# Performance work log

Hardware: AMD Instinct MI355X
Metric: run time of the kernel (lower is better)

The kernel has to match this reference:

```python
import jax, jax.numpy as jnp
import numpy as np

B, L, D, H, UNITS = 64, 4096, 512, 512, 256

def setup_inputs() -> dict:
    key = jax.random.key(0)
    ks = jax.random.split(key, 8)
    s = lambda fan_in: 1.0 / np.sqrt(fan_in)
    return {
        "features": jax.random.normal(ks[0], (B, L, D), dtype=jnp.float32),
        "hidden": jax.random.normal(ks[1], (B, H), dtype=jnp.float32),
        "W1_k": jax.random.uniform(ks[2], (D, UNITS), jnp.float32, -s(D), s(D)),
        "W1_b": jnp.zeros((UNITS,), jnp.float32),
        "W2_k": jax.random.uniform(ks[3], (H, UNITS), jnp.float32, -s(H), s(H)),
        "W2_b": jnp.zeros((UNITS,), jnp.float32),
        "V_k": jax.random.uniform(ks[4], (UNITS, 1), jnp.float32, -s(UNITS), s(UNITS)),
        "V_b": jnp.zeros((1,), jnp.float32),
    }

def reference(features, hidden, W1_k, W1_b, W2_k, W2_b, V_k, V_b):
    # features: [B, L, D], hidden: [B, H]
    f_proj = jnp.einsum('bld,du->blu', features, W1_k) + W1_b          # [B, L, U]
    h_proj = (hidden @ W2_k + W2_b)[:, None, :]                        # [B, 1, U]
    score = jnp.einsum('blu,uo->blo', jnp.tanh(f_proj + h_proj), V_k) + V_b  # [B, L, 1]
    attention_weights = jax.nn.softmax(score, axis=1)                  # [B, L, 1]
    context_vector = jnp.sum(attention_weights * features, axis=1)     # [B, D]
    return (context_vector, attention_weights)
```

## Files before the change

### kernel.cpp

```cpp
#include <hip/hip_runtime.h>

#define Bsz 64
#define Lsz 4096
#define Dsz 512
#define Hsz 512
#define Usz 256
#define LT  64
#define NLB (Lsz / LT)
#define AW  520

typedef __attribute__((ext_vector_type(8))) short s8v;
typedef __attribute__((ext_vector_type(4))) float f4v;
typedef __attribute__((ext_vector_type(8))) unsigned short u16x8;

__device__ __forceinline__ unsigned short f2bf(float f) {
    unsigned int u = __float_as_uint(f);
    u += 0x7FFFu + ((u >> 16) & 1u);
    return (unsigned short)(u >> 16);
}
__device__ __forceinline__ float bf2f(unsigned int lo16) {
    return __uint_as_float(lo16 << 16);
}


__global__ __launch_bounds__(256) void k_prep(const float* __restrict__ W1,
                                              const float* __restrict__ hidden,
                                              const float* __restrict__ W2,
                                              unsigned short* __restrict__ W1T,
                                              float* __restrict__ hp_part,
                                              float* __restrict__ den,
                                              float* __restrict__ ctx_acc) {
    int blk = blockIdx.x, tid = threadIdx.x;
    if (blk < 32) {
        __shared__ unsigned short Lt[64][72];
        int kb = blk >> 2, ub = blk & 3;
        {
            int rr = tid >> 2, c16 = (tid & 3) * 16;
            const float* src = W1 + (size_t)(kb * 64 + rr) * Usz + ub * 64 + c16;
            f4v v0 = *reinterpret_cast<const f4v*>(src);
            f4v v1 = *reinterpret_cast<const f4v*>(src + 4);
            f4v v2 = *reinterpret_cast<const f4v*>(src + 8);
            f4v v3 = *reinterpret_cast<const f4v*>(src + 12);
            u16x8 o0 = { f2bf(v0.x), f2bf(v0.y), f2bf(v0.z), f2bf(v0.w),
                         f2bf(v1.x), f2bf(v1.y), f2bf(v1.z), f2bf(v1.w) };
            u16x8 o1 = { f2bf(v2.x), f2bf(v2.y), f2bf(v2.z), f2bf(v2.w),
                         f2bf(v3.x), f2bf(v3.y), f2bf(v3.z), f2bf(v3.w) };
            *reinterpret_cast<u16x8*>(&Lt[rr][c16])     = o0;
            *reinterpret_cast<u16x8*>(&Lt[rr][c16 + 8]) = o1;
        }
        __syncthreads();
        {
            int ur = tid >> 2, k16 = (tid & 3) * 16;
            u16x8 o0, o1;
#pragma unroll
            for (int i = 0; i < 8; ++i) o0[i] = Lt[k16 + i][ur];
#pragma unroll
            for (int i = 0; i < 8; ++i) o1[i] = Lt[k16 + 8 + i][ur];
            unsigned short* dst = W1T + (size_t)(ub * 64 + ur) * Dsz + kb * 64 + k16;
            *reinterpret_cast<u16x8*>(dst)     = o0;
            *reinterpret_cast<u16x8*>(dst + 8) = o1;
        }
    } else if (blk < 288) {
        int idx = blk - 32;
        int kq = idx >> 6, b = idx & 63;
        const float* hrow = hidden + (size_t)b * Hsz + kq * 128;
        const float* w2p  = W2 + (size_t)(kq * 128) * Usz + tid;
        float a0 = 0.f, a1 = 0.f, a2 = 0.f, a3 = 0.f;
#pragma unroll 8
        for (int k = 0; k < 128; k += 4) {
            a0 = fmaf(hrow[k + 0], w2p[(size_t)(k + 0) * Usz], a0);
            a1 = fmaf(hrow[k + 1], w2p[(size_t)(k + 1) * Usz], a1);
            a2 = fmaf(hrow[k + 2], w2p[(size_t)(k + 2) * Usz], a2);
            a3 = fmaf(hrow[k + 3], w2p[(size_t)(k + 3) * Usz], a3);
        }
        hp_part[((size_t)kq * Bsz + b) * Usz + tid] = (a0 + a1) + (a2 + a3);
    } else {
        int b = blk - 288;
        if (tid == 0) den[b] = 0.f;
        ctx_acc[b * Dsz + tid] = 0.f;
        ctx_acc[b * Dsz + 256 + tid] = 0.f;
    }
}

__global__ void __launch_bounds__(512)
__attribute__((amdgpu_waves_per_eu(4, 4))) k_score_ctx(
    const float* __restrict__ feat, const unsigned short* __restrict__ W1T,
    const float* __restrict__ hp_part, const float* __restrict__ W1b,
    const float* __restrict__ W2b, const float* __restrict__ Vk,
    const float* __restrict__ Vb, float* __restrict__ el_arr,
    float* __restrict__ den, float* __restrict__ ctx_acc)
{
    __shared__ __align__(16) unsigned short A[LT][AW];
    __shared__ float hp[Usz], vv[Usz];
    __shared__ float spart[8][LT];
    __shared__ float el[LT];
    __shared__ float pc[2][Dsz];

    const int tid  = threadIdx.x;
    const int w    = tid >> 6;
    const int lane = tid & 63;
    const int lr   = lane & 15;
    const int lg   = lane >> 4;
    const int b    = blockIdx.x >> 6;
    const int lb   = blockIdx.x & 63;
    const int l0   = lb * LT;

    if (tid < Usz) {
        const float* hpb = hp_part + (size_t)b * Usz + tid;
        hp[tid] = (hpb[0] + hpb[Bsz * Usz]) + (hpb[2 * Bsz * Usz] + hpb[3 * Bsz * Usz])
                + W1b[tid] + W2b[tid];
        vv[tid] = Vk[tid];
    }

    {
        const float* fb = feat + ((size_t)b * Lsz + l0) * Dsz;
        const int c8 = (tid & 63) * 8;
#pragma unroll 2
        for (int i = 0; i < 8; ++i) {
            int row = i * 8 + w;
            const float* rp = fb + (size_t)row * Dsz + c8;
            f4v v0 = *reinterpret_cast<const f4v*>(rp);
            f4v v1 = *reinterpret_cast<const f4v*>(rp + 4);
            u16x8 o = { f2bf(v0.x), f2bf(v0.y), f2bf(v0.z), f2bf(v0.w),
                        f2bf(v1.x), f2bf(v1.y), f2bf(v1.z), f2bf(v1.w) };
            *reinterpret_cast<u16x8*>(&A[row][c8]) = o;
        }
    }
    __syncthreads();

    const unsigned short* bp0 = W1T + (size_t)(w * 32 + lr) * Dsz + lg * 8;
    const unsigned short* bp1 = bp0 + 16 * Dsz;
    f4v acc[4][2];
#pragma unroll
    for (int mf = 0; mf < 4; ++mf) {
        acc[mf][0] = (f4v){0.f, 0.f, 0.f, 0.f};
        acc[mf][1] = (f4v){0.f, 0.f, 0.f, 0.f};
    }

    s8v bq[4][2];
#pragma unroll
    for (int i = 0; i < 4; ++i) {
        bq[i][0] = *reinterpret_cast<const s8v*>(bp0 + i * 32);
        bq[i][1] = *reinterpret_cast<const s8v*>(bp1 + i * 32);
    }

#pragma unroll
    for (int ks = 0; ks < 16; ++ks) {
        s8v c0 = bq[ks & 3][0];
        s8v c1 = bq[ks & 3][1];
        if (ks < 12) {
            bq[ks & 3][0] = *reinterpret_cast<const s8v*>(bp0 + (ks + 4) * 32);
            bq[ks & 3][1] = *reinterpret_cast<const s8v*>(bp1 + (ks + 4) * 32);
        }
        const int kof = ks * 32 + lg * 8;
#pragma unroll
        for (int mf = 0; mf < 4; ++mf) {
            s8v a = *reinterpret_cast<const s8v*>(&A[mf * 16 + lr][kof]);
            acc[mf][0] = __builtin_amdgcn_mfma_f32_16x16x32_bf16(a, c0, acc[mf][0], 0, 0, 0);
            acc[mf][1] = __builtin_amdgcn_mfma_f32_16x16x32_bf16(a, c1, acc[mf][1], 0, 0, 0);
        }
    }

    {
        float rs[4][4];
#pragma unroll
        for (int mf = 0; mf < 4; ++mf)
#pragma unroll
            for (int r = 0; r < 4; ++r) rs[mf][r] = 0.f;
#pragma unroll
        for (int mf = 0; mf < 4; ++mf)
#pragma unroll
            for (int nf = 0; nf < 2; ++nf) {
                int col = w * 32 + nf * 16 + lr;
                float hpv = hp[col], vvv = vv[col];
#pragma unroll
                for (int r = 0; r < 4; ++r) {
                    float x = acc[mf][nf][r] + hpv;
                    float e = __expf(2.f * x);
                    rs[mf][r] = fmaf(1.f - 2.f / (e + 1.f), vvv, rs[mf][r]);
                }
            }
#pragma unroll
        for (int off = 1; off < 16; off <<= 1)
#pragma unroll
            for (int mf = 0; mf < 4; ++mf)
#pragma unroll
                for (int r = 0; r < 4; ++r)
                    rs[mf][r] += __shfl_xor(rs[mf][r], off, 64);
        if (lr == 0)
#pragma unroll
            for (int mf = 0; mf < 4; ++mf)
#pragma unroll
                for (int r = 0; r < 4; ++r)
                    spart[w][mf * 16 + lg * 4 + r] = rs[mf][r];
    }
    __syncthreads();

    if (tid < LT) {
        float s = Vb[0];
#pragma unroll
        for (int ww = 0; ww < 8; ++ww) s += spart[ww][tid];
        float e = __expf(s);
        el[tid] = e;
        el_arr[(size_t)b * Lsz + l0 + tid] = e;
        float es = e;
#pragma unroll
        for (int off = 1; off < 64; off <<= 1) es += __shfl_xor(es, off, 64);
        if (tid == 0) atomicAdd(&den[b], es);
    }
    __syncthreads();

    {
        const int qr = tid >> 8;
        const int d0 = (tid & 255) * 2;
        float a0 = 0.f, a1 = 0.f;
#pragma unroll 8
        for (int li = 0; li < 32; ++li) {
            int l = qr * 32 + li;
            unsigned int pk = *reinterpret_cast<const unsigned int*>(&A[l][d0]);
            float e = el[l];
            a0 = fmaf(e, bf2f(pk & 0xFFFFu), a0);
            a1 = fmaf(e, bf2f(pk >> 16), a1);
        }
        pc[qr][d0]     = a0;
        pc[qr][d0 + 1] = a1;
    }
    __syncthreads();
    atomicAdd(&ctx_acc[b * Dsz + tid], pc[0][tid] + pc[1][tid]);
}

__global__ __launch_bounds__(256) void k_finalize(const float* __restrict__ el_arr,
                                                  const float* __restrict__ den,
                                                  const float* __restrict__ ctx_acc,
                                                  float* __restrict__ ctx,
                                                  float* __restrict__ wout) {
    int blk = blockIdx.x, tid = threadIdx.x;
    int b = blk >> 2, q = blk & 3;
    float inv = 1.f / den[b];
    size_t base = (size_t)b * Lsz + q * 1024 + tid * 4;
    f4v e4 = *reinterpret_cast<const f4v*>(&el_arr[base]);
    f4v w4 = { e4.x * inv, e4.y * inv, e4.z * inv, e4.w * inv };
    *reinterpret_cast<f4v*>(&wout[base]) = w4;
    if (tid < 128) {
        int d = q * 128 + tid;
        ctx[(size_t)b * Dsz + d] = ctx_acc[b * Dsz + d] * inv;
    }
}

extern "C" void kernel_launch(void* const* d_in, const int* in_sizes, int n_in,
                              void* d_out, int out_size, void* d_ws, size_t ws_size,
                              hipStream_t stream) {
    const float* feat   = (const float*)d_in[0];
    const float* hidden = (const float*)d_in[1];
    const float* W1     = (const float*)d_in[2];
    const float* W1b    = (const float*)d_in[3];
    const float* W2     = (const float*)d_in[4];
    const float* W2b    = (const float*)d_in[5];
    const float* Vk     = (const float*)d_in[6];
    const float* Vb     = (const float*)d_in[7];

    unsigned short* w1t = (unsigned short*)d_ws;
    float* hp_part = (float*)((char*)d_ws + 256 * 1024);
    float* el_arr  = (float*)((char*)d_ws + 512 * 1024);
    float* den     = (float*)((char*)d_ws + 1536 * 1024);
    float* ctx_acc = (float*)((char*)d_ws + 1536 * 1024 + 256);

    float* ctx  = (float*)d_out;
    float* wout = ctx + Bsz * Dsz;

    k_prep<<<352, 256, 0, stream>>>(W1, hidden, W2, w1t, hp_part, den, ctx_acc);
    k_score_ctx<<<Bsz * NLB, 512, 0, stream>>>(feat, w1t, hp_part, W1b, W2b,
                                               Vk, Vb, el_arr, den, ctx_acc);
    k_finalize<<<Bsz * 4, 256, 0, stream>>>(el_arr, den, ctx_acc, ctx, wout);
}
```

Measured before the change: 200.8 us.

## Pipeline feature tile loads in K-chunks overlapped with MFMA compute

Instead of staging the full 64x512 feature tile into LDS before any MFMA work, the kernel now loads and converts it in four 128-column chunks. The global loads for the next chunk are issued before the MFMAs on the current chunk, then converted to bf16 and written to LDS behind a barrier. The goal is to hide global memory latency behind tensor-core work. In exchange it adds three block barriers, uses sched_barrier to pin instruction order, and loads W1T per chunk rather than with a rolling prefetch.

```diff
diff --git a/kernel.cpp b/kernel.cpp
--- a/kernel.cpp
+++ b/kernel.cpp
@@ -20,6 +20,10 @@
 }
 __device__ __forceinline__ float bf2f(unsigned int lo16) {
     return __uint_as_float(lo16 << 16);
+}
+__device__ __forceinline__ void barrier_lds() {
+    asm volatile("s_waitcnt lgkmcnt(0)" ::: "memory");
+    __builtin_amdgcn_s_barrier();
 }
 
 
@@ -105,26 +109,27 @@
     const int lb   = blockIdx.x & 63;
     const int l0   = lb * LT;
 
+    const int srow = tid >> 3;
+    const int scol = (tid & 7) * 16;
+    const float* fb = feat + ((size_t)b * Lsz + l0) * Dsz + (size_t)srow * Dsz + scol;
+
+    f4v st[4];
+#pragma unroll
+    for (int i = 0; i < 4; ++i) st[i] = *reinterpret_cast<const f4v*>(fb + i * 4);
+
     if (tid < Usz) {
         const float* hpb = hp_part + (size_t)b * Usz + tid;
         hp[tid] = (hpb[0] + hpb[Bsz * Usz]) + (hpb[2 * Bsz * Usz] + hpb[3 * Bsz * Usz])
                 + W1b[tid] + W2b[tid];
         vv[tid] = Vk[tid];
     }
-
     {
-        const float* fb = feat + ((size_t)b * Lsz + l0) * Dsz;
-        const int c8 = (tid & 63) * 8;
-#pragma unroll 2
-        for (int i = 0; i < 8; ++i) {
-            int row = i * 8 + w;
-            const float* rp = fb + (size_t)row * Dsz + c8;
-            f4v v0 = *reinterpret_cast<const f4v*>(rp);
-            f4v v1 = *reinterpret_cast<const f4v*>(rp + 4);
-            u16x8 o = { f2bf(v0.x), f2bf(v0.y), f2bf(v0.z), f2bf(v0.w),
-                        f2bf(v1.x), f2bf(v1.y), f2bf(v1.z), f2bf(v1.w) };
-            *reinterpret_cast<u16x8*>(&A[row][c8]) = o;
-        }
+        u16x8 o0 = { f2bf(st[0].x), f2bf(st[0].y), f2bf(st[0].z), f2bf(st[0].w),
+                     f2bf(st[1].x), f2bf(st[1].y), f2bf(st[1].z), f2bf(st[1].w) };
+        u16x8 o1 = { f2bf(st[2].x), f2bf(st[2].y), f2bf(st[2].z), f2bf(st[2].w),
+                     f2bf(st[3].x), f2bf(st[3].y), f2bf(st[3].z), f2bf(st[3].w) };
+        *reinterpret_cast<u16x8*>(&A[srow][scol])     = o0;
+        *reinterpret_cast<u16x8*>(&A[srow][scol + 8]) = o1;
     }
     __syncthreads();
 
@@ -137,27 +142,41 @@
         acc[mf][1] = (f4v){0.f, 0.f, 0.f, 0.f};
     }
 
-    s8v bq[4][2];
-#pragma unroll
-    for (int i = 0; i < 4; ++i) {
-        bq[i][0] = *reinterpret_cast<const s8v*>(bp0 + i * 32);
-        bq[i][1] = *reinterpret_cast<const s8v*>(bp1 + i * 32);
-    }
-
-#pragma unroll
-    for (int ks = 0; ks < 16; ++ks) {
-        s8v c0 = bq[ks & 3][0];
-        s8v c1 = bq[ks & 3][1];
-        if (ks < 12) {
-            bq[ks & 3][0] = *reinterpret_cast<const s8v*>(bp0 + (ks + 4) * 32);
-            bq[ks & 3][1] = *reinterpret_cast<const s8v*>(bp1 + (ks + 4) * 32);
-        }
-        const int kof = ks * 32 + lg * 8;
-#pragma unroll
-        for (int mf = 0; mf < 4; ++mf) {
-            s8v a = *reinterpret_cast<const s8v*>(&A[mf * 16 + lr][kof]);
-            acc[mf][0] = __builtin_amdgcn_mfma_f32_16x16x32_bf16(a, c0, acc[mf][0], 0, 0, 0);
-            acc[mf][1] = __builtin_amdgcn_mfma_f32_16x16x32_bf16(a, c1, acc[mf][1], 0, 0, 0);
+#pragma unroll
+    for (int c = 0; c < 4; ++c) {
+        s8v bq[4][2];
+#pragma unroll
+        for (int k = 0; k < 4; ++k) {
+            bq[k][0] = *reinterpret_cast<const s8v*>(bp0 + (c * 4 + k) * 32);
+            bq[k][1] = *reinterpret_cast<const s8v*>(bp1 + (c * 4 + k) * 32);
+        }
+        __builtin_amdgcn_sched_barrier(0);
+        if (c < 3) {
+#pragma unroll
+            for (int i = 0; i < 4; ++i)
+                st[i] = *reinterpret_cast<const f4v*>(fb + (c + 1) * 128 + i * 4);
+        }
+        __builtin_amdgcn_sched_barrier(0);
+#pragma unroll
+        for (int k = 0; k < 4; ++k) {
+            const int kof = (c * 4 + k) * 32 + lg * 8;
+#pragma unroll
+            for (int mf = 0; mf < 4; ++mf) {
+                s8v a = *reinterpret_cast<const s8v*>(&A[mf * 16 + lr][kof]);
+                acc[mf][0] = __builtin_amdgcn_mfma_f32_16x16x32_bf16(a, bq[k][0], acc[mf][0], 0, 0, 0);
+                acc[mf][1] = __builtin_amdgcn_mfma_f32_16x16x32_bf16(a, bq[k][1], acc[mf][1], 0, 0, 0);
+            }
+        }
+        __builtin_amdgcn_sched_barrier(0);
+        if (c < 3) {
+            const int cc = (c + 1) * 128 + scol;
+            u16x8 o0 = { f2bf(st[0].x), f2bf(st[0].y), f2bf(st[0].z), f2bf(st[0].w),
+                         f2bf(st[1].x), f2bf(st[1].y), f2bf(st[1].z), f2bf(st[1].w) };
+            u16x8 o1 = { f2bf(st[2].x), f2bf(st[2].y), f2bf(st[2].z), f2bf(st[2].w),
+                         f2bf(st[3].x), f2bf(st[3].y), f2bf(st[3].z), f2bf(st[3].w) };
+            *reinterpret_cast<u16x8*>(&A[srow][cc])     = o0;
+            *reinterpret_cast<u16x8*>(&A[srow][cc + 8]) = o1;
+            barrier_lds();
         }
     }
 
```

Measured after the change: 190.6 us. 5.1% less time.

## Halve row tile to 32, use 256-thread blocks with XOR-swizzled LDS and double-buffered B

Applied to the files above, without the earlier changes.

Shrinks the L tile from 64 to 32 rows and the block from 512 to 256 threads, so each wave now computes a 32x64 output slab instead of 64x32. Shared-memory padding is replaced by an XOR swizzle to avoid bank conflicts while cutting LDS size. B fragments are double-buffered with sched_barrier so the next k-step's global loads are issued ahead of the current MFMAs. The context reduction drops the second partial buffer and its barrier, at the cost of twice as many blocks and twice as many global atomics on ctx_acc and den.

```diff
diff --git a/kernel.cpp b/kernel.cpp
--- a/kernel.cpp
+++ b/kernel.cpp
@@ -5,13 +5,15 @@
 #define Dsz 512
 #define Hsz 512
 #define Usz 256
-#define LT  64
+#define LT  32
 #define NLB (Lsz / LT)
-#define AW  520
 
 typedef __attribute__((ext_vector_type(8))) short s8v;
 typedef __attribute__((ext_vector_type(4))) float f4v;
+typedef __attribute__((ext_vector_type(2))) float f2v;
 typedef __attribute__((ext_vector_type(8))) unsigned short u16x8;
+
+#define SW(r, c) (((((c) >> 3) ^ ((r) & 7)) << 3) | ((c) & 7))
 
 __device__ __forceinline__ unsigned short f2bf(float f) {
     unsigned int u = __float_as_uint(f);
@@ -82,30 +84,58 @@
     }
 }
 
-__global__ void __launch_bounds__(512)
-__attribute__((amdgpu_waves_per_eu(4, 4))) k_score_ctx(
+#define LOADB(dst, ks)                                                         \
+    {                                                                          \
+        dst[0] = *reinterpret_cast<const s8v*>(bp0 + (ks) * 32);               \
+        dst[1] = *reinterpret_cast<const s8v*>(bp0 + 8192  + (ks) * 32);       \
+        dst[2] = *reinterpret_cast<const s8v*>(bp0 + 16384 + (ks) * 32);       \
+        dst[3] = *reinterpret_cast<const s8v*>(bp0 + 24576 + (ks) * 32);       \
+    }
+
+#define GEMM1(ks, cur)                                                         \
+    {                                                                          \
+        const int kof = (ks) * 32 + lg * 8;                                    \
+        s8v a0 = *reinterpret_cast<const s8v*>(&A[lr][SW(lr, kof)]);           \
+        s8v a1 = *reinterpret_cast<const s8v*>(&A[16 + lr][SW(16 + lr, kof)]); \
+        acc[0][0] = __builtin_amdgcn_mfma_f32_16x16x32_bf16(a0, cur[0], acc[0][0], 0, 0, 0); \
+        acc[0][1] = __builtin_amdgcn_mfma_f32_16x16x32_bf16(a0, cur[1], acc[0][1], 0, 0, 0); \
+        acc[0][2] = __builtin_amdgcn_mfma_f32_16x16x32_bf16(a0, cur[2], acc[0][2], 0, 0, 0); \
+        acc[0][3] = __builtin_amdgcn_mfma_f32_16x16x32_bf16(a0, cur[3], acc[0][3], 0, 0, 0); \
+        acc[1][0] = __builtin_amdgcn_mfma_f32_16x16x32_bf16(a1, cur[0], acc[1][0], 0, 0, 0); \
+        acc[1][1] = __builtin_amdgcn_mfma_f32_16x16x32_bf16(a1, cur[1], acc[1][1], 0, 0, 0); \
+        acc[1][2] = __builtin_amdgcn_mfma_f32_16x16x32_bf16(a1, cur[2], acc[1][2], 0, 0, 0); \
+        acc[1][3] = __builtin_amdgcn_mfma_f32_16x16x32_bf16(a1, cur[3], acc[1][3], 0, 0, 0); \
+    }
+
+#define GROUP(ks, cur, nxt)                                                    \
+    {                                                                          \
+        if ((ks) < 15) LOADB(nxt, (ks) + 1);                                   \
+        __builtin_amdgcn_sched_barrier(0);                                     \
+        GEMM1(ks, cur);                                                        \
+    }
+
+__global__ __launch_bounds__(256, 4) void k_score_ctx(
     const float* __restrict__ feat, const unsigned short* __restrict__ W1T,
     const float* __restrict__ hp_part, const float* __restrict__ W1b,
     const float* __restrict__ W2b, const float* __restrict__ Vk,
     const float* __restrict__ Vb, float* __restrict__ el_arr,
     float* __restrict__ den, float* __restrict__ ctx_acc)
 {
-    __shared__ __align__(16) unsigned short A[LT][AW];
+    __shared__ __align__(16) unsigned short A[LT][Dsz];
     __shared__ float hp[Usz], vv[Usz];
-    __shared__ float spart[8][LT];
+    __shared__ float spart[4][LT];
     __shared__ float el[LT];
-    __shared__ float pc[2][Dsz];
 
     const int tid  = threadIdx.x;
     const int w    = tid >> 6;
     const int lane = tid & 63;
     const int lr   = lane & 15;
     const int lg   = lane >> 4;
-    const int b    = blockIdx.x >> 6;
-    const int lb   = blockIdx.x & 63;
+    const int b    = blockIdx.x >> 7;
+    const int lb   = blockIdx.x & 127;
     const int l0   = lb * LT;
 
-    if (tid < Usz) {
+    {
         const float* hpb = hp_part + (size_t)b * Usz + tid;
         hp[tid] = (hpb[0] + hpb[Bsz * Usz]) + (hpb[2 * Bsz * Usz] + hpb[3 * Bsz * Usz])
                 + W1b[tid] + W2b[tid];
@@ -113,65 +143,53 @@
     }
 
     {
-        const float* fb = feat + ((size_t)b * Lsz + l0) * Dsz;
-        const int c8 = (tid & 63) * 8;
-#pragma unroll 2
-        for (int i = 0; i < 8; ++i) {
-            int row = i * 8 + w;
-            const float* rp = fb + (size_t)row * Dsz + c8;
-            f4v v0 = *reinterpret_cast<const f4v*>(rp);
-            f4v v1 = *reinterpret_cast<const f4v*>(rp + 4);
-            u16x8 o = { f2bf(v0.x), f2bf(v0.y), f2bf(v0.z), f2bf(v0.w),
-                        f2bf(v1.x), f2bf(v1.y), f2bf(v1.z), f2bf(v1.w) };
-            *reinterpret_cast<u16x8*>(&A[row][c8]) = o;
+        const int row = tid >> 3;
+        const int cb  = (tid & 7) * 16;
+        const float* fp = feat + ((size_t)b * Lsz + l0 + row) * Dsz + cb;
+#pragma unroll
+        for (int j = 0; j < 4; ++j) {
+            f4v s0 = *reinterpret_cast<const f4v*>(fp + j * 128);
+            f4v s1 = *reinterpret_cast<const f4v*>(fp + j * 128 + 4);
+            f4v s2 = *reinterpret_cast<const f4v*>(fp + j * 128 + 8);
+            f4v s3 = *reinterpret_cast<const f4v*>(fp + j * 128 + 12);
+            u16x8 o = { f2bf(s0.x), f2bf(s0.y), f2bf(s0.z), f2bf(s0.w),
+                        f2bf(s1.x), f2bf(s1.y), f2bf(s1.z), f2bf(s1.w) };
+            u16x8 p = { f2bf(s2.x), f2bf(s2.y), f2bf(s2.z), f2bf(s2.w),
+                        f2bf(s3.x), f2bf(s3.y), f2bf(s3.z), f2bf(s3.w) };
+            const int sc = j * 128 + cb;
+            *reinterpret_cast<u16x8*>(&A[row][SW(row, sc)])     = o;
+            *reinterpret_cast<u16x8*>(&A[row][SW(row, sc + 8)]) = p;
         }
     }
     __syncthreads();
 
-    const unsigned short* bp0 = W1T + (size_t)(w * 32 + lr) * Dsz + lg * 8;
-    const unsigned short* bp1 = bp0 + 16 * Dsz;
-    f4v acc[4][2];
-#pragma unroll
-    for (int mf = 0; mf < 4; ++mf) {
-        acc[mf][0] = (f4v){0.f, 0.f, 0.f, 0.f};
-        acc[mf][1] = (f4v){0.f, 0.f, 0.f, 0.f};
-    }
-
-    s8v bq[4][2];
-#pragma unroll
-    for (int i = 0; i < 4; ++i) {
-        bq[i][0] = *reinterpret_cast<const s8v*>(bp0 + i * 32);
-        bq[i][1] = *reinterpret_cast<const s8v*>(bp1 + i * 32);
-    }
-
-#pragma unroll
-    for (int ks = 0; ks < 16; ++ks) {
-        s8v c0 = bq[ks & 3][0];
-        s8v c1 = bq[ks & 3][1];
-        if (ks < 12) {
-            bq[ks & 3][0] = *reinterpret_cast<const s8v*>(bp0 + (ks + 4) * 32);
-            bq[ks & 3][1] = *reinterpret_cast<const s8v*>(bp1 + (ks + 4) * 32);
-        }
-        const int kof = ks * 32 + lg * 8;
-#pragma unroll
-        for (int mf = 0; mf < 4; ++mf) {
-            s8v a = *reinterpret_cast<const s8v*>(&A[mf * 16 + lr][kof]);
-            acc[mf][0] = __builtin_amdgcn_mfma_f32_16x16x32_bf16(a, c0, acc[mf][0], 0, 0, 0);
-            acc[mf][1] = __builtin_amdgcn_mfma_f32_16x16x32_bf16(a, c1, acc[mf][1], 0, 0, 0);
-        }
-    }
-
-    {
-        float rs[4][4];
-#pragma unroll
-        for (int mf = 0; mf < 4; ++mf)
+    const unsigned short* bp0 = W1T + (size_t)(w * 64 + lr) * Dsz + lg * 8;
+    f4v acc[2][4];
+#pragma unroll
+    for (int mf = 0; mf < 2; ++mf)
+#pragma unroll
+        for (int nf = 0; nf < 4; ++nf) acc[mf][nf] = (f4v){0.f, 0.f, 0.f, 0.f};
+
+    {
+        s8v ba[4], bb[4];
+        LOADB(ba, 0);
+        GROUP(0,  ba, bb); GROUP(1,  bb, ba); GROUP(2,  ba, bb); GROUP(3,  bb, ba);
+        GROUP(4,  ba, bb); GROUP(5,  bb, ba); GROUP(6,  ba, bb); GROUP(7,  bb, ba);
+        GROUP(8,  ba, bb); GROUP(9,  bb, ba); GROUP(10, ba, bb); GROUP(11, bb, ba);
+        GROUP(12, ba, bb); GROUP(13, bb, ba); GROUP(14, ba, bb); GROUP(15, bb, ba);
+    }
+
+    {
+        float rs[2][4];
+#pragma unroll
+        for (int mf = 0; mf < 2; ++mf)
 #pragma unroll
             for (int r = 0; r < 4; ++r) rs[mf][r] = 0.f;
 #pragma unroll
-        for (int mf = 0; mf < 4; ++mf)
-#pragma unroll
-            for (int nf = 0; nf < 2; ++nf) {
-                int col = w * 32 + nf * 16 + lr;
+        for (int mf = 0; mf < 2; ++mf)
+#pragma unroll
+            for (int nf = 0; nf < 4; ++nf) {
+                int col = w * 64 + nf * 16 + lr;
                 float hpv = hp[col], vvv = vv[col];
 #pragma unroll
                 for (int r = 0; r < 4; ++r) {
@@ -183,13 +201,13 @@
 #pragma unroll
         for (int off = 1; off < 16; off <<= 1)
 #pragma unroll
-            for (int mf = 0; mf < 4; ++mf)
+            for (int mf = 0; mf < 2; ++mf)
 #pragma unroll
                 for (int r = 0; r < 4; ++r)
                     rs[mf][r] += __shfl_xor(rs[mf][r], off, 64);
         if (lr == 0)
 #pragma unroll
-            for (int mf = 0; mf < 4; ++mf)
+            for (int mf = 0; mf < 2; ++mf)
 #pragma unroll
                 for (int r = 0; r < 4; ++r)
                     spart[w][mf * 16 + lg * 4 + r] = rs[mf][r];
@@ -197,36 +215,30 @@
     __syncthreads();
 
     if (tid < LT) {
-        float s = Vb[0];
-#pragma unroll
-        for (int ww = 0; ww < 8; ++ww) s += spart[ww][tid];
+        float s = Vb[0] + (spart[0][tid] + spart[1][tid]) + (spart[2][tid] + spart[3][tid]);
         float e = __expf(s);
         el[tid] = e;
         el_arr[(size_t)b * Lsz + l0 + tid] = e;
         float es = e;
 #pragma unroll
-        for (int off = 1; off < 64; off <<= 1) es += __shfl_xor(es, off, 64);
+        for (int off = 1; off < 32; off <<= 1) es += __shfl_xor(es, off, 64);
         if (tid == 0) atomicAdd(&den[b], es);
     }
     __syncthreads();
 
     {
-        const int qr = tid >> 8;
-        const int d0 = (tid & 255) * 2;
-        float a0 = 0.f, a1 = 0.f;
+        const int d0 = tid * 2;
+        float c0 = 0.f, c1 = 0.f;
 #pragma unroll 8
-        for (int li = 0; li < 32; ++li) {
-            int l = qr * 32 + li;
-            unsigned int pk = *reinterpret_cast<const unsigned int*>(&A[l][d0]);
+        for (int l = 0; l < LT; ++l) {
+            unsigned int pk = *reinterpret_cast<const unsigned int*>(&A[l][SW(l, d0)]);
             float e = el[l];
-            a0 = fmaf(e, bf2f(pk & 0xFFFFu), a0);
-            a1 = fmaf(e, bf2f(pk >> 16), a1);
-        }
-        pc[qr][d0]     = a0;
-        pc[qr][d0 + 1] = a1;
-    }
-    __syncthreads();
-    atomicAdd(&ctx_acc[b * Dsz + tid], pc[0][tid] + pc[1][tid]);
+            c0 = fmaf(e, bf2f(pk & 0xFFFFu), c0);
+            c1 = fmaf(e, bf2f(pk >> 16), c1);
+        }
+        atomicAdd(&ctx_acc[b * Dsz + d0],     c0);
+        atomicAdd(&ctx_acc[b * Dsz + d0 + 1], c1);
+    }
 }
 
 __global__ __launch_bounds__(256) void k_finalize(const float* __restrict__ el_arr,
@@ -269,7 +281,7 @@
     float* wout = ctx + Bsz * Dsz;
 
     k_prep<<<352, 256, 0, stream>>>(W1, hidden, W2, w1t, hp_part, den, ctx_acc);
-    k_score_ctx<<<Bsz * NLB, 512, 0, stream>>>(feat, w1t, hp_part, W1b, W2b,
+    k_score_ctx<<<Bsz * NLB, 256, 0, stream>>>(feat, w1t, hp_part, W1b, W2b,
                                                Vk, Vb, el_arr, den, ctx_acc);
     k_finalize<<<Bsz * 4, 256, 0, stream>>>(el_arr, den, ctx_acc, ctx, wout);
 }
```

After: 319.6 us. 1.59x slower.
